# Kernel optimization log

Hardware: AMD Instinct MI355X
Metric: run time of the kernel (lower is better)

## Reference

```python
import jax, jax.numpy as jnp
import numpy as np

EMBED = 256
HEADS = 8
LEVELS = 4
POINTS = 8  # total points per level; POINTS // D offsets per z-anchor
CAMS = 6
BS = 1
NQ = 4096   # 64x64 BEV grid
D = 4       # z anchors
SHAPES = np.array([[92, 160], [46, 80], [23, 40], [12, 20]], dtype=np.int64)  # (H, W) per level
L = int((SHAPES[:, 0] * SHAPES[:, 1]).sum())  # 19560
HEAD_DIM = EMBED // HEADS


def setup_inputs() -> dict:
    key = jax.random.key(0)
    ks = jax.random.split(key, 12)
    lsi = np.concatenate([[0], np.cumsum(SHAPES[:, 0] * SHAPES[:, 1])[:-1]]).astype(np.int64)
    s = 1.0 / np.sqrt(EMBED)
    return {
        'query': jax.random.normal(ks[0], (BS, NQ, EMBED), jnp.float32),
        'key_feat': jax.random.normal(ks[1], (CAMS, L, BS, EMBED), jnp.float32),
        'value_feat': jax.random.normal(ks[2], (CAMS, L, BS, EMBED), jnp.float32),
        'reference_points_cam': jax.random.uniform(ks[3], (CAMS, BS, NQ, D, 2), jnp.float32),
        'bev_mask': jax.random.bernoulli(ks[4], 0.3, (CAMS, BS, NQ, D)),
        'spatial_shapes': jnp.asarray(SHAPES),
        'level_start_index': jnp.asarray(lsi),
        'W_value': jax.random.normal(ks[5], (EMBED, EMBED), jnp.float32) * s,
        'b_value': jnp.zeros((EMBED,), jnp.float32),
        'W_off': jax.random.normal(ks[6], (EMBED, HEADS * LEVELS * POINTS * 2), jnp.float32) * 0.01,
        'b_off': jax.random.normal(ks[7], (HEADS * LEVELS * POINTS * 2,), jnp.float32) * 0.5,
        'W_attn': jax.random.normal(ks[8], (EMBED, HEADS * LEVELS * POINTS), jnp.float32) * 0.02,
        'b_attn': jnp.zeros((HEADS * LEVELS * POINTS,), jnp.float32),
        'W_out': jax.random.normal(ks[9], (EMBED, EMBED), jnp.float32) * s,
        'b_out': jnp.zeros((EMBED,), jnp.float32),
    }


def _sample_level(vl, locs, H, W):
    # Bilinear sampling == F.grid_sample(bilinear, zeros, align_corners=False) with grid = 2*loc-1.
    # vl: (B, H*W, heads, d); locs: (B, nq, heads, P, 2) normalized to [0,1].
    B, nq, heads, P, _ = locs.shape
    x = locs[..., 0] * W - 0.5
    y = locs[..., 1] * H - 0.5
    x0 = jnp.floor(x)
    y0 = jnp.floor(y)
    lx = x - x0
    ly = y - y0
    x0i = x0.astype(jnp.int32)
    y0i = y0.astype(jnp.int32)
    out = jnp.zeros((B, nq, heads, P, vl.shape[-1]), vl.dtype)
    corners = ((0, 0, (1 - lx) * (1 - ly)), (1, 0, lx * (1 - ly)),
               (0, 1, (1 - lx) * ly), (1, 1, lx * ly))
    for dx, dy, w in corners:
        xi = x0i + dx
        yi = y0i + dy
        valid = (xi >= 0) & (xi < W) & (yi >= 0) & (yi < H)
        idx = jnp.clip(yi, 0, H - 1) * W + jnp.clip(xi, 0, W - 1)  # (B,nq,heads,P)
        idx = idx.transpose(0, 1, 3, 2).reshape(B, nq * P, heads)   # (B, nq*P, heads)
        g = jnp.take_along_axis(vl, idx[..., None], axis=1)         # (B, nq*P, heads, d)
        g = g.reshape(B, nq, P, heads, -1).transpose(0, 1, 3, 2, 4)  # (B,nq,heads,P,d)
        out = out + (w * valid)[..., None] * g
    return out


def _deform_attn(q, v, ref, W_value, b_value, W_off, b_off, W_attn, b_attn):
    # MSDeformableAttention3D (BEVFormer). q: (B,nq,E), v: (B,L,E), ref: (B,nq,D,2).
    B, nq, _ = q.shape
    val = (v @ W_value + b_value).reshape(B, L, HEADS, HEAD_DIM)
    off = (q @ W_off + b_off).reshape(B, nq, HEADS, LEVELS, POINTS, 2)
    attn = jax.nn.softmax((q @ W_attn + b_attn).reshape(B, nq, HEADS, LEVELS * POINTS), axis=-1)
    attn = attn.reshape(B, nq, HEADS, LEVELS, POINTS)
    # offset_normalizer = [W, H] per level
    norm = jnp.asarray(SHAPES[:, ::-1].copy(), jnp.float32)
    off = off / norm[None, None, None, :, None, :]
    ppz = POINTS // D
    off = off.reshape(B, nq, HEADS, LEVELS, ppz, D, 2)
    loc = ref[:, :, None, None, None, :, :] + off  # (B,nq,heads,levels,ppz,D,2)
    loc = loc.reshape(B, nq, HEADS, LEVELS, POINTS, 2)
    out = jnp.zeros((B, nq, HEADS, HEAD_DIM), q.dtype)
    start = 0
    for li in range(LEVELS):
        H, W = int(SHAPES[li, 0]), int(SHAPES[li, 1])
        vl = val[:, start:start + H * W]
        s = _sample_level(vl, loc[:, :, :, li], H, W)  # (B,nq,heads,P,d)
        out = out + jnp.einsum('bqhp,bqhpd->bqhd', attn[:, :, :, li], s)
        start += H * W
    return out.reshape(B, nq, EMBED)


def reference(query, key_feat, value_feat, reference_points_cam, bev_mask,
              spatial_shapes, level_start_index,
              W_value, b_value, W_off, b_off, W_attn, b_attn, W_out, b_out):
    bs, nq, E = query.shape
    # fused_query broadcast across cameras (no dynamic cam embed)
    q = jnp.broadcast_to(query[:, None], (bs, CAMS, nq, E)).reshape(bs * CAMS, nq, E)
    v = value_feat.transpose(2, 0, 1, 3).reshape(bs * CAMS, L, E)
    ref = reference_points_cam.transpose(1, 0, 2, 3, 4).reshape(bs * CAMS, nq, D, 2)
    out = _deform_attn(q, v, ref, W_value, b_value, W_off, b_off, W_attn, b_attn)
    out = out.reshape(bs, CAMS, nq, E)
    # masked scatter-sum over cameras == torch's gather/rebatch/scatter pipeline
    hit = (bev_mask.sum(-1) > 0)                 # (cams, bs, nq)
    maskf = hit.transpose(1, 0, 2).astype(query.dtype)  # (bs, cams, nq)
    slots = (out * maskf[..., None]).sum(axis=1)        # (bs, nq, E)
    count = jnp.maximum(maskf.sum(axis=1), 1.0)
    slots = slots / count[..., None]
    slots = slots @ W_out + b_out
    return slots + query  # dropout in eval mode == identity
```

## Files before the change

### kernel.cpp

```cpp
#include <hip/hip_runtime.h>
#include <hip/hip_bf16.h>

#define NQ 4096
#define EMBED 256
#define HEADS 8
#define HEAD_DIM 32
#define LEVELS 4
#define POINTS 8
#define CAMS 6
#define LTOT 19560
#define MROWS (CAMS * LTOT)

using bf16x8 = __attribute__((ext_vector_type(8))) __bf16;
using f32x4v = __attribute__((ext_vector_type(4))) float;
using f32x2v = __attribute__((ext_vector_type(2))) float;

__device__ inline ushort f2bf(float f) {
    unsigned u = __builtin_bit_cast(unsigned, f);
    u += 0x7FFFu + ((u >> 16) & 1u);
    return (ushort)(u >> 16);
}
__device__ inline float bflo(unsigned u) {
    return __builtin_bit_cast(float, u << 16);
}
__device__ inline float bfhi(unsigned u) {
    return __builtin_bit_cast(float, u & 0xFFFF0000u);
}
__device__ inline float bpermf(int addr, float v) {
    return __builtin_bit_cast(float, __builtin_amdgcn_ds_bpermute(addr, __builtin_bit_cast(int, v)));
}
__device__ inline unsigned bpermu(int addr, unsigned v) {
    return (unsigned)__builtin_amdgcn_ds_bpermute(addr, (int)v);
}
__device__ inline unsigned char f2fp8(float f) {
    return (unsigned char)(__builtin_amdgcn_cvt_pk_fp8_f32(f, 0.f, 0, false) & 0xFF);
}

__global__ __launch_bounds__(256) void detect_kernel(const unsigned int* __restrict__ bm,
                                                     unsigned int* __restrict__ flag) {
    __shared__ unsigned int red[256];
    const int t = threadIdx.x;
    unsigned int acc = 0;
    for (int i = t; i < (CAMS * NQ * 4) / 4; i += 256)
        acc |= (bm[i] & 0xFFFFFF00u);
    red[t] = acc;
    __syncthreads();
    for (int s = 128; s > 0; s >>= 1) {
        if (t < s) red[t] |= red[t + s];
        __syncthreads();
    }
    if (t == 0) flag[0] = red[0] ? 1u : 0u;
}

__global__ __launch_bounds__(256) void mask_kernel(const void* __restrict__ bm,
                                                   const unsigned int* __restrict__ flag,
                                                   float* __restrict__ maskf,
                                                   float* __restrict__ countf) {
    const int q = blockIdx.x * 256 + threadIdx.x;
    if (q >= NQ) return;
    const bool u8 = (flag[0] != 0);
    float cnt = 0.f;
    #pragma unroll
    for (int c = 0; c < CAMS; c++) {
        bool hit;
        if (u8) {
            const unsigned int w = ((const unsigned int*)bm)[c * NQ + q];
            hit = (w != 0);
        } else {
            const int* p = (const int*)bm;
            int s = 0;
            #pragma unroll
            for (int d = 0; d < 4; d++) s |= p[(c * NQ + q) * 4 + d];
            hit = (s != 0);
        }
        maskf[c * NQ + q] = hit ? 1.f : 0.f;
        cnt += hit ? 1.f : 0.f;
    }
    countf[q] = fmaxf(cnt, 1.f);
}

__global__ __launch_bounds__(256) void wtall_kernel(const float* __restrict__ W_off,
                                                    const float* __restrict__ W_attn,
                                                    const float* __restrict__ W_out,
                                                    const float* __restrict__ W_value,
                                                    ushort* __restrict__ WTall) {
    __shared__ float tile[32][33];
    const int bn = blockIdx.x;
    const int bk = blockIdx.y;
    const int t = threadIdx.x;
    const int r = t >> 5, c = t & 31;
    #pragma unroll
    for (int it = 0; it < 4; it++) {
        const int k = bk * 32 + it * 8 + r;
        const int n = bn * 32 + c;
        float v;
        if (n < 512)       v = W_off[(size_t)k * 512 + n];
        else if (n < 768)  v = W_attn[(size_t)k * 256 + (n - 512)];
        else if (n < 1024) v = W_out[(size_t)k * 256 + (n - 768)];
        else               v = W_value[(size_t)k * 256 + (n - 1024)];
        tile[it * 8 + r][c] = v;
    }
    __syncthreads();
    #pragma unroll
    for (int it = 0; it < 4; it++) {
        const int n = bn * 32 + it * 8 + r;
        const int k = bk * 32 + c;
        WTall[(size_t)n * 256 + k] = f2bf(tile[c][it * 8 + r]);
    }
}

#define LDT 40

__global__ __launch_bounds__(256) void proj_gemm(const float* __restrict__ A,
                                                 const ushort* __restrict__ WT,
                                                 float* __restrict__ C) {
    __shared__ ushort As[128 * LDT];
    __shared__ ushort Bs[128 * LDT];
    const int t = threadIdx.x;
    const int wave = t >> 6, lane = t & 63;
    const int wm = (wave & 1) * 64, wn = (wave >> 1) * 64;
    const int n0 = blockIdx.x * 128, m0 = blockIdx.y * 128;
    const int fl = lane & 15, fk = (lane >> 4) * 8;
    const int sr = t >> 1, sk = (t & 1) * 16;

    const float*  arow = A  + (size_t)(m0 + sr) * 256;
    const ushort* brow = WT + (size_t)(n0 + sr) * 256;

    f32x4v acc[4][4];
    #pragma unroll
    for (int i = 0; i < 4; i++)
        #pragma unroll
        for (int j = 0; j < 4; j++) acc[i][j] = (f32x4v)(0.f);

    for (int k0 = 0; k0 < 256; k0 += 32) {
        bf16x8 w0, w1;
        #pragma unroll
        for (int u = 0; u < 2; u++) {
            const float4 v = *(const float4*)&arow[k0 + sk + u * 4];
            w0[u * 4 + 0] = (__bf16)v.x; w0[u * 4 + 1] = (__bf16)v.y;
            w0[u * 4 + 2] = (__bf16)v.z; w0[u * 4 + 3] = (__bf16)v.w;
        }
        #pragma unroll
        for (int u = 0; u < 2; u++) {
            const float4 v = *(const float4*)&arow[k0 + sk + 8 + u * 4];
            w1[u * 4 + 0] = (__bf16)v.x; w1[u * 4 + 1] = (__bf16)v.y;
            w1[u * 4 + 2] = (__bf16)v.z; w1[u * 4 + 3] = (__bf16)v.w;
        }
        *(bf16x8*)&As[sr * LDT + sk]     = w0;
        *(bf16x8*)&As[sr * LDT + sk + 8] = w1;
        const uint4* bp = (const uint4*)&brow[k0 + sk];
        *(uint4*)&Bs[sr * LDT + sk]     = bp[0];
        *(uint4*)&Bs[sr * LDT + sk + 8] = bp[1];
        __syncthreads();

        bf16x8 af[4], bfv[4];
        #pragma unroll
        for (int i = 0; i < 4; i++)
            af[i] = *(const bf16x8*)&As[(wm + i * 16 + fl) * LDT + fk];
        #pragma unroll
        for (int j = 0; j < 4; j++)
            bfv[j] = *(const bf16x8*)&Bs[(wn + j * 16 + fl) * LDT + fk];
        #pragma unroll
        for (int i = 0; i < 4; i++)
            #pragma unroll
            for (int j = 0; j < 4; j++)
                acc[i][j] = __builtin_amdgcn_mfma_f32_16x16x32_bf16(af[i], bfv[j], acc[i][j], 0, 0, 0);
        __syncthreads();
    }

    const int rb = (lane >> 4) * 4;
    #pragma unroll
    for (int j = 0; j < 4; j++) {
        const int col = n0 + wn + j * 16 + fl;
        #pragma unroll
        for (int i = 0; i < 4; i++)
            #pragma unroll
            for (int r = 0; r < 4; r++)
                C[(size_t)(m0 + wm + i * 16 + rb + r) * 768 + col] = acc[i][j][r];
    }
}

__global__ __launch_bounds__(256) void proj_epi(const float* __restrict__ logits,
                                                const float* __restrict__ b_off,
                                                const float* __restrict__ b_attn,
                                                float* __restrict__ offn,
                                                float* __restrict__ attnw) {
    const int t = threadIdx.x;
    const int q0 = blockIdx.x * 4;
    const float Wl[4] = {160.f, 80.f, 40.f, 20.f};
    const float Hl[4] = {92.f, 46.f, 23.f, 12.f};
    const int j0 = t, j1 = t + 256;
    const int l0 = (j0 & 63) >> 4, l1 = (j1 & 63) >> 4;
    const float inv0 = 1.0f / ((j0 & 1) ? Hl[l0] : Wl[l0]);
    const float inv1 = 1.0f / ((j1 & 1) ? Hl[l1] : Wl[l1]);
    const float bo0 = b_off[j0], bo1 = b_off[j1], ba = b_attn[t];
    #pragma unroll
    for (int i = 0; i < 4; i++) {
        const float* lg = logits + (size_t)(q0 + i) * 768;
        offn[(size_t)(q0 + i) * 512 + j0] = (lg[j0] + bo0) * inv0;
        offn[(size_t)(q0 + i) * 512 + j1] = (lg[j1] + bo1) * inv1;
        const float v = lg[512 + t] + ba;
        float m = v;
        for (int s = 16; s > 0; s >>= 1) m = fmaxf(m, __shfl_xor(m, s, 32));
        const float e = expf(v - m);
        float ssum = e;
        for (int s = 16; s > 0; s >>= 1) ssum += __shfl_xor(ssum, s, 32);
        attnw[(size_t)(q0 + i) * 256 + t] = e / ssum;
    }
}

__global__ __launch_bounds__(256) void gemm_mfma(const float* __restrict__ A,
                                                 const ushort* __restrict__ WT,
                                                 const float* __restrict__ bias,
                                                 unsigned char* __restrict__ C, int M) {
    __shared__ ushort As[128 * LDT];
    __shared__ ushort Bs[128 * LDT];
    const int t = threadIdx.x;
    const int wave = t >> 6, lane = t & 63;
    const int wm = (wave & 1) * 64, wn = (wave >> 1) * 64;
    const int n0 = blockIdx.x * 128, m0 = blockIdx.y * 128;
    const int fl = lane & 15, fk = (lane >> 4) * 8;
    const int sr = t >> 1, sk = (t & 1) * 16;

    int ar = m0 + sr; if (ar >= M) ar = M - 1;
    const float*  arow = A  + (size_t)ar * 256;
    const ushort* brow = WT + (size_t)(n0 + sr) * 256;

    f32x4v acc[4][4];
    #pragma unroll
    for (int i = 0; i < 4; i++)
        #pragma unroll
        for (int j = 0; j < 4; j++) acc[i][j] = (f32x4v)(0.f);

    for (int k0 = 0; k0 < 256; k0 += 32) {
        bf16x8 w0, w1;
        #pragma unroll
        for (int u = 0; u < 2; u++) {
            const float4 v = *(const float4*)&arow[k0 + sk + u * 4];
            w0[u * 4 + 0] = (__bf16)v.x; w0[u * 4 + 1] = (__bf16)v.y;
            w0[u * 4 + 2] = (__bf16)v.z; w0[u * 4 + 3] = (__bf16)v.w;
        }
        #pragma unroll
        for (int u = 0; u < 2; u++) {
            const float4 v = *(const float4*)&arow[k0 + sk + 8 + u * 4];
            w1[u * 4 + 0] = (__bf16)v.x; w1[u * 4 + 1] = (__bf16)v.y;
            w1[u * 4 + 2] = (__bf16)v.z; w1[u * 4 + 3] = (__bf16)v.w;
        }
        *(bf16x8*)&As[sr * LDT + sk]     = w0;
        *(bf16x8*)&As[sr * LDT + sk + 8] = w1;
        const uint4* bp = (const uint4*)&brow[k0 + sk];
        *(uint4*)&Bs[sr * LDT + sk]     = bp[0];
        *(uint4*)&Bs[sr * LDT + sk + 8] = bp[1];
        __syncthreads();

        bf16x8 af[4], bfv[4];
        #pragma unroll
        for (int i = 0; i < 4; i++)
            af[i] = *(const bf16x8*)&As[(wm + i * 16 + fl) * LDT + fk];
        #pragma unroll
        for (int j = 0; j < 4; j++)
            bfv[j] = *(const bf16x8*)&Bs[(wn + j * 16 + fl) * LDT + fk];
        #pragma unroll
        for (int i = 0; i < 4; i++)
            #pragma unroll
            for (int j = 0; j < 4; j++)
                acc[i][j] = __builtin_amdgcn_mfma_f32_16x16x32_bf16(af[i], bfv[j], acc[i][j], 0, 0, 0);
        __syncthreads();
    }

    const int rb = (lane >> 4) * 4;
    #pragma unroll
    for (int j = 0; j < 4; j++) {
        const int col = n0 + wn + j * 16 + fl;
        const float bv = bias[col];
        #pragma unroll
        for (int i = 0; i < 4; i++) {
            #pragma unroll
            for (int r = 0; r < 4; r++) {
                const int row = m0 + wm + i * 16 + rb + r;
                if (row < M)
                    C[(size_t)row * 256 + col] = f2fp8(acc[i][j][r] + bv);
            }
        }
    }
}

__device__ __forceinline__ void bperm_batch(int aP0, int aP1,
                                            const float* wts, const unsigned* rowB,
                                            float* w, unsigned* ro) {
    #pragma unroll
    for (int c = 0; c < 4; c++) {
        w[c]     = bpermf(aP0, wts[c]);
        ro[c]    = bpermu(aP0, rowB[c]);
        w[4 + c] = bpermf(aP1, wts[c]);
        ro[4 + c] = bpermu(aP1, rowB[c]);
    }
}
__device__ __forceinline__ void load_batch8(const char* base, const unsigned* ro, unsigned* vv) {
    #pragma unroll
    for (int c = 0; c < 8; c++)
        vv[c] = *(const unsigned*)(base + ro[c]);
}
__device__ __forceinline__ void acc_batch8(const float* w, const unsigned* vv,
                                           float2& a01, float2& a23) {
    #pragma unroll
    for (int c = 0; c < 8; c++) {
        const float wt = w[c];
        const f32x2v lo = __builtin_amdgcn_cvt_pk_f32_fp8(vv[c], false);
        const f32x2v hi = __builtin_amdgcn_cvt_pk_f32_fp8(vv[c], true);
        a01.x += wt * lo.x; a01.y += wt * lo.y;
        a23.x += wt * hi.x; a23.y += wt * hi.y;
    }
}

__global__ __launch_bounds__(256) void sample_kernel(const float* __restrict__ refp,
                                                     const float* __restrict__ offn,
                                                     const float* __restrict__ attnw,
                                                     const unsigned char* __restrict__ val,
                                                     const float* __restrict__ maskf,
                                                     ushort* __restrict__ out_cam) {
    const int wv = threadIdx.x >> 6, lane = threadIdx.x & 63;
    const int pair = blockIdx.x * 4 + wv;
    const int cam = pair >> 12;
    const int q = pair & (NQ - 1);

    const int h = lane >> 3, dg = lane & 7;
    ushort* dst = &out_cam[((size_t)cam * NQ + q) * EMBED + h * HEAD_DIM + dg * 4];
    const float mk = maskf[cam * NQ + q];
    if (mk == 0.f) {
        ushort4 z; z.x = 0; z.y = 0; z.z = 0; z.w = 0;
        *(ushort4*)dst = z;
        return;
    }

    const unsigned hd = (unsigned)(h * HEAD_DIM + dg * 4);
    const float* refq = refp + ((size_t)cam * NQ + q) * 8;
    const float* offq = offn + (size_t)q * 512 + h * 64;
    const float* attq = attnw + (size_t)q * 256 + h * 32;
    const char* camLane = (const char*)val + (size_t)cam * (LTOT * EMBED) + hd;

    const float rx = refq[2 * (dg & 3)], ry = refq[2 * (dg & 3) + 1];
    const int grp4 = (lane & 56) * 4;

    const int Hs[4] = {92, 46, 23, 12};
    const int Ws[4] = {160, 80, 40, 20};
    const int st[4] = {0, 14720, 18400, 19320};

    float2 a01 = {0.f, 0.f}, a23 = {0.f, 0.f};
    #pragma unroll
    for (int l = 0; l < LEVELS; l++) {
        const int H = Hs[l], W = Ws[l];
        const float fW = (float)W, fH = (float)H;

        float wts[4];
        unsigned rowB[4];
        {
            const float x = (rx + offq[l * 16 + dg * 2]) * fW - 0.5f;
            const float y = (ry + offq[l * 16 + dg * 2 + 1]) * fH - 0.5f;
            const float x0f = floorf(x), y0f = floorf(y);
            const float lx = x - x0f, ly = y - y0f;
            const int x0 = (int)x0f, y0 = (int)y0f, x1 = x0 + 1, y1 = y0 + 1;
            const float aw = attq[l * 8 + dg];
            const bool vx0 = (unsigned)x0 < (unsigned)W;
            const bool vx1 = (unsigned)x1 < (unsigned)W;
            const bool vy0 = (unsigned)y0 < (unsigned)H;
            const bool vy1 = (unsigned)y1 < (unsigned)H;
            const float hx = lx * aw, gx = aw - hx;
            wts[0] = (vx0 & vy0) ? gx * (1.f - ly) : 0.f;
            wts[1] = (vx1 & vy0) ? hx * (1.f - ly) : 0.f;
            wts[2] = (vx0 & vy1) ? gx * ly : 0.f;
            wts[3] = (vx1 & vy1) ? hx * ly : 0.f;
            const int cx0 = min(max(x0, 0), W - 1), cx1 = min(max(x1, 0), W - 1);
            const int cy0 = min(max(y0, 0), H - 1), cy1 = min(max(y1, 0), H - 1);
            const unsigned r0 = (unsigned)(st[l] + cy0 * W), r1 = (unsigned)(st[l] + cy1 * W);
            rowB[0] = (r0 + cx0) * EMBED;
            rowB[1] = (r0 + cx1) * EMBED;
            rowB[2] = (r1 + cx0) * EMBED;
            rowB[3] = (r1 + cx1) * EMBED;
        }

        float w0[8], w1[8];
        unsigned ro0[8], ro1[8];
        unsigned vv0[8], vv1[8];

        bperm_batch(grp4 + 0 * 4, grp4 + 1 * 4, wts, rowB, w0, ro0);
        load_batch8(camLane, ro0, vv0);
        bperm_batch(grp4 + 2 * 4, grp4 + 3 * 4, wts, rowB, w1, ro1);
        load_batch8(camLane, ro1, vv1);
        acc_batch8(w0, vv0, a01, a23);
        bperm_batch(grp4 + 4 * 4, grp4 + 5 * 4, wts, rowB, w0, ro0);
        load_batch8(camLane, ro0, vv0);
        acc_batch8(w1, vv1, a01, a23);
        bperm_batch(grp4 + 6 * 4, grp4 + 7 * 4, wts, rowB, w1, ro1);
        load_batch8(camLane, ro1, vv1);
        acc_batch8(w0, vv0, a01, a23);
        acc_batch8(w1, vv1, a01, a23);
    }
    ushort4 o;
    o.x = __builtin_bit_cast(ushort, (__bf16)a01.x);
    o.y = __builtin_bit_cast(ushort, (__bf16)a01.y);
    o.z = __builtin_bit_cast(ushort, (__bf16)a23.x);
    o.w = __builtin_bit_cast(ushort, (__bf16)a23.y);
    *(ushort4*)dst = o;
}

__global__ __launch_bounds__(256) void mean_kernel(const ushort* __restrict__ out_cam,
                                                   const float* __restrict__ maskf,
                                                   const float* __restrict__ countf,
                                                   ushort* __restrict__ Sbf) {
    const int wv = threadIdx.x >> 6, lane = threadIdx.x & 63;
    const int q = blockIdx.x * 4 + wv;
    const int c4 = lane * 4;
    float4 acc = make_float4(0.f, 0.f, 0.f, 0.f);
    #pragma unroll
    for (int c = 0; c < CAMS; c++) {
        const float m = maskf[c * NQ + q];
        const uint2 v = *(const uint2*)&out_cam[(((size_t)c * NQ + q) << 8) + c4];
        acc.x += m * bflo(v.x); acc.y += m * bfhi(v.x);
        acc.z += m * bflo(v.y); acc.w += m * bfhi(v.y);
    }
    const float inv = 1.0f / countf[q];
    ushort4 s;
    s.x = __builtin_bit_cast(ushort, (__bf16)(acc.x * inv));
    s.y = __builtin_bit_cast(ushort, (__bf16)(acc.y * inv));
    s.z = __builtin_bit_cast(ushort, (__bf16)(acc.z * inv));
    s.w = __builtin_bit_cast(ushort, (__bf16)(acc.w * inv));
    *(ushort4*)&Sbf[(size_t)q * 256 + c4] = s;
}

__global__ __launch_bounds__(256) void out_gemm(const ushort* __restrict__ A,
                                                const ushort* __restrict__ WT,
                                                const float* __restrict__ bias,
                                                const float* __restrict__ query,
                                                float* __restrict__ out) {
    __shared__ ushort As[128 * LDT];
    __shared__ ushort Bs[128 * LDT];
    const int t = threadIdx.x;
    const int wave = t >> 6, lane = t & 63;
    const int wm = (wave & 1) * 64, wn = (wave >> 1) * 64;
    const int n0 = blockIdx.x * 128, m0 = blockIdx.y * 128;
    const int fl = lane & 15, fk = (lane >> 4) * 8;
    const int sr = t >> 1, sk = (t & 1) * 16;

    const ushort* arow = A  + (size_t)(m0 + sr) * 256;
    const ushort* brow = WT + (size_t)(n0 + sr) * 256;

    f32x4v acc[4][4];
    #pragma unroll
    for (int i = 0; i < 4; i++)
        #pragma unroll
        for (int j = 0; j < 4; j++) acc[i][j] = (f32x4v)(0.f);

    for (int k0 = 0; k0 < 256; k0 += 32) {
        const uint4* ap = (const uint4*)&arow[k0 + sk];
        *(uint4*)&As[sr * LDT + sk]     = ap[0];
        *(uint4*)&As[sr * LDT + sk + 8] = ap[1];
        const uint4* bp = (const uint4*)&brow[k0 + sk];
        *(uint4*)&Bs[sr * LDT + sk]     = bp[0];
        *(uint4*)&Bs[sr * LDT + sk + 8] = bp[1];
        __syncthreads();

        bf16x8 af[4], bfv[4];
        #pragma unroll
        for (int i = 0; i < 4; i++)
            af[i] = *(const bf16x8*)&As[(wm + i * 16 + fl) * LDT + fk];
        #pragma unroll
        for (int j = 0; j < 4; j++)
            bfv[j] = *(const bf16x8*)&Bs[(wn + j * 16 + fl) * LDT + fk];
        #pragma unroll
        for (int i = 0; i < 4; i++)
            #pragma unroll
            for (int j = 0; j < 4; j++)
                acc[i][j] = __builtin_amdgcn_mfma_f32_16x16x32_bf16(af[i], bfv[j], acc[i][j], 0, 0, 0);
        __syncthreads();
    }

    const int rb = (lane >> 4) * 4;
    #pragma unroll
    for (int j = 0; j < 4; j++) {
        const int col = n0 + wn + j * 16 + fl;
        const float bv = bias[col];
        #pragma unroll
        for (int i = 0; i < 4; i++) {
            #pragma unroll
            for (int r = 0; r < 4; r++) {
                const int row = m0 + wm + i * 16 + rb + r;
                out[(size_t)row * 256 + col] =
                    acc[i][j][r] + bv + query[(size_t)row * 256 + col];
            }
        }
    }
}

extern "C" void kernel_launch(void* const* d_in, const int* in_sizes, int n_in,
                              void* d_out, int out_size, void* d_ws, size_t ws_size,
                              hipStream_t stream) {
    const float* query      = (const float*)d_in[0];
    const float* value_feat = (const float*)d_in[2];
    const float* refp       = (const float*)d_in[3];
    const void*  bev        = d_in[4];
    const float* W_value    = (const float*)d_in[7];
    const float* b_value    = (const float*)d_in[8];
    const float* W_off      = (const float*)d_in[9];
    const float* b_off      = (const float*)d_in[10];
    const float* W_attn     = (const float*)d_in[11];
    const float* b_attn     = (const float*)d_in[12];
    const float* W_out      = (const float*)d_in[13];
    const float* b_out      = (const float*)d_in[14];

    float* ws      = (float*)d_ws;
    float* offn    = ws;
    float* attnw   = offn + 2097152;
    float* maskf   = attnw + 1048576;
    float* countf  = maskf + 24576;
    unsigned int* flag = (unsigned int*)(countf + 4096);
    float* logits  = countf + 4096 + 64;
    unsigned char* val = (unsigned char*)(logits + 3145728);
    ushort* out_cam = (ushort*)(val + (size_t)MROWS * EMBED);
    ushort* Sbf    = out_cam + (size_t)CAMS * NQ * EMBED;
    ushort* WTall  = Sbf + (size_t)NQ * EMBED;

    detect_kernel<<<1, 256, 0, stream>>>((const unsigned int*)bev, flag);
    mask_kernel<<<16, 256, 0, stream>>>(bev, flag, maskf, countf);
    wtall_kernel<<<dim3(40, 8), 256, 0, stream>>>(W_off, W_attn, W_out, W_value, WTall);
    proj_gemm<<<dim3(6, 32), 256, 0, stream>>>(query, WTall, logits);
    proj_epi<<<NQ / 4, 256, 0, stream>>>(logits, b_off, b_attn, offn, attnw);
    gemm_mfma<<<dim3(2, (MROWS + 127) / 128), 256, 0, stream>>>(
        value_feat, WTall + (size_t)1024 * 256, b_value, val, MROWS);
    sample_kernel<<<CAMS * NQ / 4, 256, 0, stream>>>(refp, offn, attnw, val, maskf, out_cam);
    mean_kernel<<<NQ / 4, 256, 0, stream>>>(out_cam, maskf, countf, Sbf);
    out_gemm<<<dim3(2, 32), 256, 0, stream>>>(Sbf, WTall + (size_t)768 * 256, b_out, query, (float*)d_out);
}
```

Measured before the change: 204.3 us.

## Restructure value GEMM: resident B tile, direct A register loads, prefetch

The value-projection GEMM now loads the whole 64x256 bf16 weight slice into shared memory once per block. Each wave reads its A fragments directly from global fp32 into registers, with a double-buffered prefetch of the next k-step, which removes the A staging through LDS and the per-iteration barriers. The N tile drops from 128 to 64, so the grid doubles in x and launch bounds request 4 blocks per CU. In exchange, each A row is now read from global memory four times, once per N block, instead of twice.

```diff
diff --git a/kernel.cpp b/kernel.cpp
--- a/kernel.cpp
+++ b/kernel.cpp
@@ -209,68 +209,82 @@
     }
 }
 
-__global__ __launch_bounds__(256) void gemm_mfma(const float* __restrict__ A,
-                                                 const ushort* __restrict__ WT,
-                                                 const float* __restrict__ bias,
-                                                 unsigned char* __restrict__ C, int M) {
-    __shared__ ushort As[128 * LDT];
-    __shared__ ushort Bs[128 * LDT];
+#define BSTR 264
+
+__global__ __launch_bounds__(256, 4) void gemm_mfma(const float* __restrict__ A,
+                                                    const ushort* __restrict__ WT,
+                                                    const float* __restrict__ bias,
+                                                    unsigned char* __restrict__ C, int M) {
+    __shared__ ushort Bs[64 * BSTR];
     const int t = threadIdx.x;
     const int wave = t >> 6, lane = t & 63;
-    const int wm = (wave & 1) * 64, wn = (wave >> 1) * 64;
-    const int n0 = blockIdx.x * 128, m0 = blockIdx.y * 128;
+    const int wm = (wave & 1) * 64, wn = (wave >> 1) * 32;
+    const int m0 = blockIdx.y * 128, n0 = blockIdx.x * 64;
     const int fl = lane & 15, fk = (lane >> 4) * 8;
-    const int sr = t >> 1, sk = (t & 1) * 16;
-
-    int ar = m0 + sr; if (ar >= M) ar = M - 1;
-    const float*  arow = A  + (size_t)ar * 256;
-    const ushort* brow = WT + (size_t)(n0 + sr) * 256;
-
-    f32x4v acc[4][4];
-    #pragma unroll
-    for (int i = 0; i < 4; i++)
-        #pragma unroll
-        for (int j = 0; j < 4; j++) acc[i][j] = (f32x4v)(0.f);
-
-    for (int k0 = 0; k0 < 256; k0 += 32) {
-        bf16x8 w0, w1;
-        #pragma unroll
-        for (int u = 0; u < 2; u++) {
-            const float4 v = *(const float4*)&arow[k0 + sk + u * 4];
-            w0[u * 4 + 0] = (__bf16)v.x; w0[u * 4 + 1] = (__bf16)v.y;
-            w0[u * 4 + 2] = (__bf16)v.z; w0[u * 4 + 3] = (__bf16)v.w;
-        }
-        #pragma unroll
-        for (int u = 0; u < 2; u++) {
-            const float4 v = *(const float4*)&arow[k0 + sk + 8 + u * 4];
-            w1[u * 4 + 0] = (__bf16)v.x; w1[u * 4 + 1] = (__bf16)v.y;
-            w1[u * 4 + 2] = (__bf16)v.z; w1[u * 4 + 3] = (__bf16)v.w;
-        }
-        *(bf16x8*)&As[sr * LDT + sk]     = w0;
-        *(bf16x8*)&As[sr * LDT + sk + 8] = w1;
-        const uint4* bp = (const uint4*)&brow[k0 + sk];
-        *(uint4*)&Bs[sr * LDT + sk]     = bp[0];
-        *(uint4*)&Bs[sr * LDT + sk + 8] = bp[1];
-        __syncthreads();
-
-        bf16x8 af[4], bfv[4];
-        #pragma unroll
-        for (int i = 0; i < 4; i++)
-            af[i] = *(const bf16x8*)&As[(wm + i * 16 + fl) * LDT + fk];
-        #pragma unroll
-        for (int j = 0; j < 4; j++)
-            bfv[j] = *(const bf16x8*)&Bs[(wn + j * 16 + fl) * LDT + fk];
-        #pragma unroll
-        for (int i = 0; i < 4; i++)
-            #pragma unroll
-            for (int j = 0; j < 4; j++)
-                acc[i][j] = __builtin_amdgcn_mfma_f32_16x16x32_bf16(af[i], bfv[j], acc[i][j], 0, 0, 0);
-        __syncthreads();
+
+    {
+        const int row = t >> 2, seg = (t & 3) * 64;
+        const ushort* src = WT + (size_t)(n0 + row) * 256 + seg;
+        ushort* dstp = &Bs[row * BSTR + seg];
+        #pragma unroll
+        for (int u = 0; u < 8; u++)
+            *(uint4*)(dstp + u * 8) = *(const uint4*)(src + u * 8);
+    }
+    __syncthreads();
+
+    const float* arow[4];
+    #pragma unroll
+    for (int i = 0; i < 4; i++) {
+        int r = m0 + wm + i * 16 + fl; if (r >= M) r = M - 1;
+        arow[i] = A + (size_t)r * 256 + fk;
+    }
+
+    f32x4v acc[4][2];
+    #pragma unroll
+    for (int i = 0; i < 4; i++) {
+        acc[i][0] = (f32x4v)(0.f);
+        acc[i][1] = (f32x4v)(0.f);
+    }
+
+    float4 pa[2][4][2];
+    #pragma unroll
+    for (int i = 0; i < 4; i++) {
+        pa[0][i][0] = *(const float4*)(arow[i]);
+        pa[0][i][1] = *(const float4*)(arow[i] + 4);
+    }
+
+    #pragma unroll
+    for (int ks = 0; ks < 8; ks++) {
+        const int cur = ks & 1, nxt = cur ^ 1;
+        const int k0 = ks * 32;
+        if (ks < 7) {
+            #pragma unroll
+            for (int i = 0; i < 4; i++) {
+                pa[nxt][i][0] = *(const float4*)(arow[i] + k0 + 32);
+                pa[nxt][i][1] = *(const float4*)(arow[i] + k0 + 36);
+            }
+        }
+        bf16x8 af[4];
+        #pragma unroll
+        for (int i = 0; i < 4; i++) {
+            const float4 lo = pa[cur][i][0], hi = pa[cur][i][1];
+            af[i][0] = (__bf16)lo.x; af[i][1] = (__bf16)lo.y;
+            af[i][2] = (__bf16)lo.z; af[i][3] = (__bf16)lo.w;
+            af[i][4] = (__bf16)hi.x; af[i][5] = (__bf16)hi.y;
+            af[i][6] = (__bf16)hi.z; af[i][7] = (__bf16)hi.w;
+        }
+        const bf16x8 b0 = *(const bf16x8*)&Bs[(wn + fl) * BSTR + k0 + fk];
+        const bf16x8 b1 = *(const bf16x8*)&Bs[(wn + 16 + fl) * BSTR + k0 + fk];
+        #pragma unroll
+        for (int i = 0; i < 4; i++) {
+            acc[i][0] = __builtin_amdgcn_mfma_f32_16x16x32_bf16(af[i], b0, acc[i][0], 0, 0, 0);
+            acc[i][1] = __builtin_amdgcn_mfma_f32_16x16x32_bf16(af[i], b1, acc[i][1], 0, 0, 0);
+        }
     }
 
     const int rb = (lane >> 4) * 4;
     #pragma unroll
-    for (int j = 0; j < 4; j++) {
+    for (int j = 0; j < 2; j++) {
         const int col = n0 + wn + j * 16 + fl;
         const float bv = bias[col];
         #pragma unroll
@@ -525,7 +539,7 @@
     wtall_kernel<<<dim3(40, 8), 256, 0, stream>>>(W_off, W_attn, W_out, W_value, WTall);
     proj_gemm<<<dim3(6, 32), 256, 0, stream>>>(query, WTall, logits);
     proj_epi<<<NQ / 4, 256, 0, stream>>>(logits, b_off, b_attn, offn, attnw);
-    gemm_mfma<<<dim3(2, (MROWS + 127) / 128), 256, 0, stream>>>(
+    gemm_mfma<<<dim3(4, (MROWS + 127) / 128), 256, 0, stream>>>(
         value_feat, WTall + (size_t)1024 * 256, b_value, val, MROWS);
     sample_kernel<<<CAMS * NQ / 4, 256, 0, stream>>>(refp, offn, attnw, val, maskf, out_cam);
     mean_kernel<<<NQ / 4, 256, 0, stream>>>(out_cam, maskf, countf, Sbf);
```

Result: slower. 274.2 us (+34.2%).

## Prefetch next K-slice into registers and swizzle value GEMM block order

Applied to the files above, without the earlier changes.

The value-projection GEMM now loads the next 32-wide K slice of A and B into registers while MFMAs run on the current slice, hiding global load latency behind compute. The 2D grid becomes a 1D grid with a swizzle that groups 8 M-tiles with both N halves, so the two blocks sharing the same A rows run close together and reuse them in L2. Launch bounds also request 3 blocks per CU. Prefetch registers raise register pressure, which could conflict with the occupancy hint.

```diff
diff --git a/kernel.cpp b/kernel.cpp
--- a/kernel.cpp
+++ b/kernel.cpp
@@ -209,16 +209,22 @@
     }
 }
 
-__global__ __launch_bounds__(256) void gemm_mfma(const float* __restrict__ A,
-                                                 const ushort* __restrict__ WT,
-                                                 const float* __restrict__ bias,
-                                                 unsigned char* __restrict__ C, int M) {
+__global__ __launch_bounds__(256, 3) void gemm_mfma(const float* __restrict__ A,
+                                                    const ushort* __restrict__ WT,
+                                                    const float* __restrict__ bias,
+                                                    unsigned char* __restrict__ C, int M) {
     __shared__ ushort As[128 * LDT];
     __shared__ ushort Bs[128 * LDT];
     const int t = threadIdx.x;
     const int wave = t >> 6, lane = t & 63;
     const int wm = (wave & 1) * 64, wn = (wave >> 1) * 64;
-    const int n0 = blockIdx.x * 128, m0 = blockIdx.y * 128;
+
+    const int w = blockIdx.x;
+    int mt, nh;
+    if (w < 1824) { mt = (w >> 4) * 8 + (w & 7); nh = (w >> 3) & 1; }
+    else          { mt = 912 + ((w - 1824) >> 1); nh = (w - 1824) & 1; }
+    const int m0 = mt * 128, n0 = nh * 128;
+
     const int fl = lane & 15, fk = (lane >> 4) * 8;
     const int sr = t >> 1, sk = (t & 1) * 16;
 
@@ -232,26 +238,36 @@
         #pragma unroll
         for (int j = 0; j < 4; j++) acc[i][j] = (f32x4v)(0.f);
 
-    for (int k0 = 0; k0 < 256; k0 += 32) {
+    float4 pa0 = *(const float4*)&arow[sk];
+    float4 pa1 = *(const float4*)&arow[sk + 4];
+    float4 pa2 = *(const float4*)&arow[sk + 8];
+    float4 pa3 = *(const float4*)&arow[sk + 12];
+    uint4  pb0 = *(const uint4*)&brow[sk];
+    uint4  pb1 = *(const uint4*)&brow[sk + 8];
+
+    #pragma unroll
+    for (int ks = 0; ks < 8; ks++) {
+        const int k0 = ks * 32;
         bf16x8 w0, w1;
-        #pragma unroll
-        for (int u = 0; u < 2; u++) {
-            const float4 v = *(const float4*)&arow[k0 + sk + u * 4];
-            w0[u * 4 + 0] = (__bf16)v.x; w0[u * 4 + 1] = (__bf16)v.y;
-            w0[u * 4 + 2] = (__bf16)v.z; w0[u * 4 + 3] = (__bf16)v.w;
-        }
-        #pragma unroll
-        for (int u = 0; u < 2; u++) {
-            const float4 v = *(const float4*)&arow[k0 + sk + 8 + u * 4];
-            w1[u * 4 + 0] = (__bf16)v.x; w1[u * 4 + 1] = (__bf16)v.y;
-            w1[u * 4 + 2] = (__bf16)v.z; w1[u * 4 + 3] = (__bf16)v.w;
-        }
+        w0[0] = (__bf16)pa0.x; w0[1] = (__bf16)pa0.y; w0[2] = (__bf16)pa0.z; w0[3] = (__bf16)pa0.w;
+        w0[4] = (__bf16)pa1.x; w0[5] = (__bf16)pa1.y; w0[6] = (__bf16)pa1.z; w0[7] = (__bf16)pa1.w;
+        w1[0] = (__bf16)pa2.x; w1[1] = (__bf16)pa2.y; w1[2] = (__bf16)pa2.z; w1[3] = (__bf16)pa2.w;
+        w1[4] = (__bf16)pa3.x; w1[5] = (__bf16)pa3.y; w1[6] = (__bf16)pa3.z; w1[7] = (__bf16)pa3.w;
         *(bf16x8*)&As[sr * LDT + sk]     = w0;
         *(bf16x8*)&As[sr * LDT + sk + 8] = w1;
-        const uint4* bp = (const uint4*)&brow[k0 + sk];
-        *(uint4*)&Bs[sr * LDT + sk]     = bp[0];
-        *(uint4*)&Bs[sr * LDT + sk + 8] = bp[1];
-        __syncthreads();
+        *(uint4*)&Bs[sr * LDT + sk]     = pb0;
+        *(uint4*)&Bs[sr * LDT + sk + 8] = pb1;
+        __syncthreads();
+
+        if (ks < 7) {
+            const int kn = k0 + 32;
+            pa0 = *(const float4*)&arow[kn + sk];
+            pa1 = *(const float4*)&arow[kn + sk + 4];
+            pa2 = *(const float4*)&arow[kn + sk + 8];
+            pa3 = *(const float4*)&arow[kn + sk + 12];
+            pb0 = *(const uint4*)&brow[kn + sk];
+            pb1 = *(const uint4*)&brow[kn + sk + 8];
+        }
 
         bf16x8 af[4], bfv[4];
         #pragma unroll
@@ -525,7 +541,7 @@
     wtall_kernel<<<dim3(40, 8), 256, 0, stream>>>(W_off, W_attn, W_out, W_value, WTall);
     proj_gemm<<<dim3(6, 32), 256, 0, stream>>>(query, WTall, logits);
     proj_epi<<<NQ / 4, 256, 0, stream>>>(logits, b_off, b_attn, offn, attnw);
-    gemm_mfma<<<dim3(2, (MROWS + 127) / 128), 256, 0, stream>>>(
+    gemm_mfma<<<1834, 256, 0, stream>>>(
         value_feat, WTall + (size_t)1024 * 256, b_value, val, MROWS);
     sample_kernel<<<CAMS * NQ / 4, 256, 0, stream>>>(refp, offn, attnw, val, maskf, out_cam);
     mean_kernel<<<NQ / 4, 256, 0, stream>>>(out_cam, maskf, countf, Sbf);
```

After: 190.6 us. -6.7%, faster.

## Restructure value-projection GEMM with full-K A tile, swizzled LDS, double-buffered B

Applied to the files above, without the earlier changes.

The value projection GEMM now uses 64-row M tiles. Each block loads its whole 64x256 A slab into LDS once, converted to bf16 with an XOR swizzle to avoid bank conflicts. The B panel is streamed in 32-wide K chunks through a double buffer, with the next chunk prefetched during the MFMAs. The grid is flattened, and block indices are remapped so that groups of 8 M-tiles share both N halves, which should improve L2 reuse of the fp32 A rows. The intent is to cut per-iteration sync stalls and redundant global traffic. The cost is a larger LDS footprint per block and more blocks.

```diff
diff --git a/kernel.cpp b/kernel.cpp
--- a/kernel.cpp
+++ b/kernel.cpp
@@ -209,62 +209,87 @@
     }
 }
 
+#define GMT 64
+
 __global__ __launch_bounds__(256) void gemm_mfma(const float* __restrict__ A,
                                                  const ushort* __restrict__ WT,
                                                  const float* __restrict__ bias,
                                                  unsigned char* __restrict__ C, int M) {
-    __shared__ ushort As[128 * LDT];
-    __shared__ ushort Bs[128 * LDT];
+    __shared__ ushort AsF[GMT * 256];
+    __shared__ ushort Bsb[2][128 * 32];
     const int t = threadIdx.x;
     const int wave = t >> 6, lane = t & 63;
-    const int wm = (wave & 1) * 64, wn = (wave >> 1) * 64;
-    const int n0 = blockIdx.x * 128, m0 = blockIdx.y * 128;
+    const int wm = (wave & 1) * 32, wn = (wave >> 1) * 64;
+
+    const int w = blockIdx.x;
+    int mt, nh;
+    if (w < 3664) { mt = (w >> 4) * 8 + (w & 7); nh = (w >> 3) & 1; }
+    else          { mt = 1832 + ((w - 3664) >> 1); nh = (w - 3664) & 1; }
+    const int m0 = mt * GMT, n0 = nh * 128;
+
     const int fl = lane & 15, fk = (lane >> 4) * 8;
-    const int sr = t >> 1, sk = (t & 1) * 16;
-
-    int ar = m0 + sr; if (ar >= M) ar = M - 1;
-    const float*  arow = A  + (size_t)ar * 256;
-    const ushort* brow = WT + (size_t)(n0 + sr) * 256;
-
-    f32x4v acc[4][4];
-    #pragma unroll
-    for (int i = 0; i < 4; i++)
+
+    #pragma unroll 4
+    for (int r = 0; r < 16; r++) {
+        const int e = r * 1024 + t * 4;
+        const int row = e >> 8;
+        int gr = m0 + row; if (gr >= M) gr = M - 1;
+        const float4 v = *(const float4*)&A[(size_t)gr * 256 + (e & 255)];
+        uint2 pk;
+        pk.x = (unsigned)f2bf(v.x) | ((unsigned)f2bf(v.y) << 16);
+        pk.y = (unsigned)f2bf(v.z) | ((unsigned)f2bf(v.w) << 16);
+        *(uint2*)&AsF[e ^ ((row & 7) << 3)] = pk;
+    }
+
+    const int rr = t >> 1, off = (t & 1) * 16;
+    const ushort* bsrc = WT + (size_t)(n0 + rr) * 256 + off;
+    const int bsw = (rr & 3) << 3;
+    {
+        const uint4 b0 = *(const uint4*)(bsrc);
+        const uint4 b1 = *(const uint4*)(bsrc + 8);
+        *(uint4*)&Bsb[0][(rr * 32 + off + 0) ^ bsw] = b0;
+        *(uint4*)&Bsb[0][(rr * 32 + off + 8) ^ bsw] = b1;
+    }
+    __syncthreads();
+
+    f32x4v acc[2][4];
+    #pragma unroll
+    for (int i = 0; i < 2; i++)
         #pragma unroll
         for (int j = 0; j < 4; j++) acc[i][j] = (f32x4v)(0.f);
 
-    for (int k0 = 0; k0 < 256; k0 += 32) {
-        bf16x8 w0, w1;
-        #pragma unroll
-        for (int u = 0; u < 2; u++) {
-            const float4 v = *(const float4*)&arow[k0 + sk + u * 4];
-            w0[u * 4 + 0] = (__bf16)v.x; w0[u * 4 + 1] = (__bf16)v.y;
-            w0[u * 4 + 2] = (__bf16)v.z; w0[u * 4 + 3] = (__bf16)v.w;
-        }
-        #pragma unroll
-        for (int u = 0; u < 2; u++) {
-            const float4 v = *(const float4*)&arow[k0 + sk + 8 + u * 4];
-            w1[u * 4 + 0] = (__bf16)v.x; w1[u * 4 + 1] = (__bf16)v.y;
-            w1[u * 4 + 2] = (__bf16)v.z; w1[u * 4 + 3] = (__bf16)v.w;
-        }
-        *(bf16x8*)&As[sr * LDT + sk]     = w0;
-        *(bf16x8*)&As[sr * LDT + sk + 8] = w1;
-        const uint4* bp = (const uint4*)&brow[k0 + sk];
-        *(uint4*)&Bs[sr * LDT + sk]     = bp[0];
-        *(uint4*)&Bs[sr * LDT + sk + 8] = bp[1];
-        __syncthreads();
-
-        bf16x8 af[4], bfv[4];
-        #pragma unroll
-        for (int i = 0; i < 4; i++)
-            af[i] = *(const bf16x8*)&As[(wm + i * 16 + fl) * LDT + fk];
-        #pragma unroll
-        for (int j = 0; j < 4; j++)
-            bfv[j] = *(const bf16x8*)&Bs[(wn + j * 16 + fl) * LDT + fk];
-        #pragma unroll
-        for (int i = 0; i < 4; i++)
+    #pragma unroll
+    for (int ks = 0; ks < 8; ks++) {
+        const int cur = ks & 1;
+        const int k0 = ks * 32;
+
+        uint4 nb0, nb1;
+        if (ks < 7) {
+            nb0 = *(const uint4*)(bsrc + (k0 + 32));
+            nb1 = *(const uint4*)(bsrc + (k0 + 32) + 8);
+        }
+
+        bf16x8 af[2], bfv[4];
+        #pragma unroll
+        for (int i = 0; i < 2; i++) {
+            const int row = wm + i * 16 + fl;
+            af[i] = *(const bf16x8*)&AsF[(row * 256 + k0 + fk) ^ ((fl & 7) << 3)];
+        }
+        #pragma unroll
+        for (int j = 0; j < 4; j++) {
+            const int br = wn + j * 16 + fl;
+            bfv[j] = *(const bf16x8*)&Bsb[cur][(br * 32 + fk) ^ ((fl & 3) << 3)];
+        }
+        #pragma unroll
+        for (int i = 0; i < 2; i++)
             #pragma unroll
             for (int j = 0; j < 4; j++)
                 acc[i][j] = __builtin_amdgcn_mfma_f32_16x16x32_bf16(af[i], bfv[j], acc[i][j], 0, 0, 0);
+
+        if (ks < 7) {
+            *(uint4*)&Bsb[cur ^ 1][(rr * 32 + off + 0) ^ bsw] = nb0;
+            *(uint4*)&Bsb[cur ^ 1][(rr * 32 + off + 8) ^ bsw] = nb1;
+        }
         __syncthreads();
     }
 
@@ -274,7 +299,7 @@
         const int col = n0 + wn + j * 16 + fl;
         const float bv = bias[col];
         #pragma unroll
-        for (int i = 0; i < 4; i++) {
+        for (int i = 0; i < 2; i++) {
             #pragma unroll
             for (int r = 0; r < 4; r++) {
                 const int row = m0 + wm + i * 16 + rb + r;
@@ -525,7 +550,7 @@
     wtall_kernel<<<dim3(40, 8), 256, 0, stream>>>(W_off, W_attn, W_out, W_value, WTall);
     proj_gemm<<<dim3(6, 32), 256, 0, stream>>>(query, WTall, logits);
     proj_epi<<<NQ / 4, 256, 0, stream>>>(logits, b_off, b_attn, offn, attnw);
-    gemm_mfma<<<dim3(2, (MROWS + 127) / 128), 256, 0, stream>>>(
+    gemm_mfma<<<3668, 256, 0, stream>>>(
         value_feat, WTall + (size_t)1024 * 256, b_value, val, MROWS);
     sample_kernel<<<CAMS * NQ / 4, 256, 0, stream>>>(refp, offn, attnw, val, maskf, out_cam);
     mean_kernel<<<NQ / 4, 256, 0, stream>>>(out_cam, maskf, countf, Sbf);
```

Result: faster. 198.1 us (-3.0%).
